# Kernel tuning notes

Hardware: AMD Instinct MI355X
Metric: run time of the kernel (lower is better)

## Reference

```python
import jax, jax.numpy as jnp
import numpy as np


def setup_inputs() -> dict:
    key = jax.random.key(0)
    ks = jax.random.split(key, 7)
    B, D, K, L = 32768, 256, 8, 4
    s = 1.0 / np.sqrt(D)
    return {
        "x": jax.random.normal(ks[0], (B, D), jnp.float32),
        "gate_W": jax.random.normal(ks[1], (D, K), jnp.float32) * s,
        "gate_b": jax.random.normal(ks[2], (K,), jnp.float32) * s,
        "block_W": jax.random.normal(ks[3], (L, K, D, D), jnp.float32) * s,
        "block_b": jax.random.normal(ks[4], (L, K, D), jnp.float32) * s,
        "out_W": jax.random.normal(ks[5], (K, D, D), jnp.float32) * s,
        "out_b": jax.random.normal(ks[6], (K, D), jnp.float32) * s,
    }


def _moie_block(x, alpha, W, b):
    # x: (B, in), alpha: (B, K), W: (K, in, out), b: (K, out)
    z = jnp.einsum('bi,kio->bko', x, W) + b[None]        # (B, K, out)
    return jnp.einsum('bk,bko->bo', alpha, z)            # alpha-weighted sum over experts


def reference(x, gate_W, gate_b, block_W, block_b, out_W, out_b):
    # standard gating: softmax(Linear(x)); same alpha reused at every layer
    alpha = jax.nn.softmax(x @ gate_W + gate_b, axis=-1)  # (B, K)
    h = x
    num_layers = block_W.shape[0]
    for i in range(num_layers):
        h = jax.nn.relu(_moie_block(h, alpha, block_W[i], block_b[i]))
    # output block, no activation
    return _moie_block(h, alpha, out_W, out_b)
```

## Files before the change

kernel.cpp:

```cpp
#include <hip/hip_runtime.h>
#include <hip/hip_bf16.h>

typedef __attribute__((ext_vector_type(8))) _Float16 h8v;
typedef __attribute__((ext_vector_type(4))) float f4v;

__device__ __forceinline__ ushort f16bits(float f) {
    _Float16 h = (_Float16)f;
    return __builtin_bit_cast(unsigned short, h);
}

#define GL2LDS16(g, l) __builtin_amdgcn_global_load_lds( \
    (const __attribute__((address_space(1))) void*)(g),  \
    (__attribute__((address_space(3))) void*)(l), 16, 0, 0)

#define VMCNT4() asm volatile("s_waitcnt vmcnt(4)" ::: "memory")
#define VMCNT0() asm volatile("s_waitcnt vmcnt(0)" ::: "memory")
#define LGKM0()  asm volatile("s_waitcnt lgkmcnt(0)" ::: "memory")
#define BAR()    asm volatile("s_barrier" ::: "memory")

__global__ __launch_bounds__(256) void gate_kernel(
    const float* __restrict__ x, const float* __restrict__ gW,
    const float* __restrict__ gb, float* __restrict__ alpha)
{
    int lane = threadIdx.x & 63;
    int wave = threadIdx.x >> 6;
    int row = blockIdx.x * 4 + wave;
    float4 xv = *(const float4*)(x + (size_t)row * 256 + lane * 4);
    const float* xp = (const float*)&xv;
    float p[8];
#pragma unroll
    for (int k = 0; k < 8; ++k) p[k] = 0.f;
#pragma unroll
    for (int j = 0; j < 4; ++j) {
        float xs = xp[j];
        const float* wr = gW + (lane * 4 + j) * 8;
#pragma unroll
        for (int k = 0; k < 8; ++k) p[k] = fmaf(xs, wr[k], p[k]);
    }
#pragma unroll
    for (int off = 32; off > 0; off >>= 1) {
#pragma unroll
        for (int k = 0; k < 8; ++k) p[k] += __shfl_xor(p[k], off);
    }
    float m = -1e30f;
#pragma unroll
    for (int k = 0; k < 8; ++k) { p[k] += gb[k]; m = fmaxf(m, p[k]); }
    float s = 0.f;
#pragma unroll
    for (int k = 0; k < 8; ++k) { p[k] = expf(p[k] - m); s += p[k]; }
    if (lane < 8) alpha[(size_t)row * 8 + lane] = p[lane] / s;
}

__global__ __launch_bounds__(256) void prep_weights(
    const float* __restrict__ blockW, const float* __restrict__ outW,
    ushort* __restrict__ Wh)
{
    int mat = blockIdx.x >> 4;
    int tile = blockIdx.x & 15;
    int i0 = (tile >> 2) * 64, o0 = (tile & 3) * 64;
    const float* src = (mat < 32) ? (blockW + (size_t)mat * 65536)
                                  : (outW + (size_t)(mat - 32) * 65536);
    __shared__ float tl[64][65];
    int r = threadIdx.x >> 2, c0 = (threadIdx.x & 3) * 16;
#pragma unroll
    for (int e = 0; e < 16; e += 4) {
        float4 v = *(const float4*)(src + (size_t)(i0 + r) * 256 + o0 + c0 + e);
        tl[r][c0 + e + 0] = v.x; tl[r][c0 + e + 1] = v.y;
        tl[r][c0 + e + 2] = v.z; tl[r][c0 + e + 3] = v.w;
    }
    __syncthreads();
    int oc = threadIdx.x >> 2, ic0 = (threadIdx.x & 3) * 16;
    uint hp[8];
#pragma unroll
    for (int e = 0; e < 16; e += 2) {
        ushort h0 = f16bits(tl[ic0 + e][oc]);
        ushort h1 = f16bits(tl[ic0 + e + 1][oc]);
        hp[e >> 1] = (uint)h0 | ((uint)h1 << 16);
    }
    size_t base = ((size_t)(mat * 256 + o0 + oc)) * 256 + i0 + ic0;
    *(uint4*)(Wh + base)     = make_uint4(hp[0], hp[1], hp[2], hp[3]);
    *(uint4*)(Wh + base + 8) = make_uint4(hp[4], hp[5], hp[6], hp[7]);
}

template<bool RELU>
__global__ __launch_bounds__(256, 2) void moie_gemm(
    const float* __restrict__ Hin, float* __restrict__ Hout,
    const ushort* __restrict__ Wh,
    const float* __restrict__ bias, const float* __restrict__ alpha)
{
    __shared__ __align__(16) ushort Ah[64 * 256];
    __shared__ __align__(16) ushort Bh[2][256 * 32];

    const int tid  = threadIdx.x;
    const int lane = tid & 63;
    const int wid  = tid >> 6;
    const int m0   = blockIdx.x * 64;
    const int wcol0 = wid * 64;
    const int kgl = lane >> 4;
    const int fr  = lane & 15;

    float areg[4][8];
#pragma unroll
    for (int im = 0; im < 4; ++im) {
        const float4* ap = (const float4*)(alpha + (size_t)(m0 + im * 16 + fr) * 8);
        float4 a0 = ap[0], a1 = ap[1];
        areg[im][0] = a0.x; areg[im][1] = a0.y; areg[im][2] = a0.z; areg[im][3] = a0.w;
        areg[im][4] = a1.x; areg[im][5] = a1.y; areg[im][6] = a1.z; areg[im][7] = a1.w;
    }

    int bgoff[4];
#pragma unroll
    for (int q = 0; q < 4; ++q) {
        int c = q * 256 + tid;
        int n = c >> 2;
        int kg = (c & 3) ^ ((n >> 1) & 3);
        bgoff[q] = n * 256 + kg * 8;
    }
    int boff[4];
#pragma unroll
    for (int in = 0; in < 4; ++in) {
        int n = wcol0 + in * 16 + fr;
        boff[in] = n * 32 + (kgl ^ ((n >> 1) & 3)) * 8;
    }

#pragma unroll
    for (int q = 0; q < 4; ++q)
        GL2LDS16(Wh + bgoff[q], &Bh[0][(q * 256 + wid * 64) * 8]);

    {
        const int r0  = tid >> 6;
        const int kk  = (tid & 63) * 4;
        const int kg  = kk >> 3;
        const int klo = kk & 7;
#pragma unroll
        for (int p = 0; p < 16; ++p) {
            int row = p * 4 + r0;
            float4 v = *(const float4*)(Hin + (size_t)(m0 + row) * 256 + kk);
            uint2 pk;
            pk.x = (uint)f16bits(v.x) | ((uint)f16bits(v.y) << 16);
            pk.y = (uint)f16bits(v.z) | ((uint)f16bits(v.w) << 16);
            *(uint2*)&Ah[row * 256 + (kg ^ (row & 7)) * 8 + klo] = pk;
        }
    }
    LGKM0();

    f4v acc[4][4];
#pragma unroll
    for (int a = 0; a < 4; ++a)
#pragma unroll
        for (int b = 0; b < 4; ++b) acc[a][b] = (f4v){0.f, 0.f, 0.f, 0.f};

    h8v afc[4];

#pragma unroll 1
    for (int t = 0; t < 64; ++t) {
        const int cur = t & 1;
        if (t < 63) {
            const int tn  = t + 1;
            const int en  = tn & 7;
            const int ki0 = (tn >> 3) * 32;
#pragma unroll
            for (int q = 0; q < 4; ++q)
                GL2LDS16(Wh + (size_t)en * 65536 + bgoff[q] + ki0,
                         &Bh[cur ^ 1][(q * 256 + wid * 64) * 8]);
            VMCNT4();
        } else {
            VMCNT0();
        }
        BAR();
        if ((t & 7) == 0) {
            const int kg0 = (t >> 3) * 4;
#pragma unroll
            for (int im = 0; im < 4; ++im) {
                int row = im * 16 + fr;
                afc[im] = *(const h8v*)&Ah[row * 256 + ((kg0 + kgl) ^ (row & 7)) * 8];
            }
        }
        const int e = t & 7;
        h8v as[4];
#pragma unroll
        for (int im = 0; im < 4; ++im) {
            _Float16 ah = (_Float16)areg[im][e];
            as[im] = afc[im] * ah;
        }
        h8v bf[4];
#pragma unroll
        for (int in = 0; in < 4; ++in)
            bf[in] = *(const h8v*)&Bh[cur][boff[in]];
        __builtin_amdgcn_s_setprio(1);
#pragma unroll
        for (int im = 0; im < 4; ++im)
#pragma unroll
            for (int in = 0; in < 4; ++in)
                acc[im][in] = __builtin_amdgcn_mfma_f32_16x16x32_f16(as[im], bf[in], acc[im][in], 0, 0, 0);
        __builtin_amdgcn_s_setprio(0);
        BAR();
    }

    float bv[4][8];
#pragma unroll
    for (int in = 0; in < 4; ++in) {
        int col = wcol0 + in * 16 + fr;
#pragma unroll
        for (int k = 0; k < 8; ++k) bv[in][k] = bias[k * 256 + col];
    }
#pragma unroll
    for (int im = 0; im < 4; ++im) {
#pragma unroll
        for (int j = 0; j < 4; ++j) {
            int row = m0 + im * 16 + kgl * 4 + j;
            const float4* ap = (const float4*)(alpha + (size_t)row * 8);
            float4 a0 = ap[0], a1 = ap[1];
            float a8[8] = {a0.x, a0.y, a0.z, a0.w, a1.x, a1.y, a1.z, a1.w};
#pragma unroll
            for (int in = 0; in < 4; ++in) {
                int col = wcol0 + in * 16 + fr;
                float be = 0.f;
#pragma unroll
                for (int k = 0; k < 8; ++k) be = fmaf(a8[k], bv[in][k], be);
                float v = acc[im][in][j] + be;
                if (RELU) v = fmaxf(v, 0.f);
                Hout[(size_t)row * 256 + col] = v;
            }
        }
    }
}

extern "C" void kernel_launch(void* const* d_in, const int* in_sizes, int n_in,
                              void* d_out, int out_size, void* d_ws, size_t ws_size,
                              hipStream_t stream)
{
    const float* x      = (const float*)d_in[0];
    const float* gW     = (const float*)d_in[1];
    const float* gb     = (const float*)d_in[2];
    const float* blockW = (const float*)d_in[3];
    const float* blockB = (const float*)d_in[4];
    const float* outW   = (const float*)d_in[5];
    const float* outB   = (const float*)d_in[6];
    float* out = (float*)d_out;

    char* ws = (char*)d_ws;
    float*  alpha = (float*)ws;
    ushort* Wh    = (ushort*)(ws + (1 << 20));

    prep_weights<<<640, 256, 0, stream>>>(blockW, outW, Wh);
    gate_kernel<<<8192, 256, 0, stream>>>(x, gW, gb, alpha);

    const size_t WL = (size_t)8 * 65536;
    moie_gemm<true ><<<512, 256, 0, stream>>>(x,   out, Wh,          blockB,            alpha);
    moie_gemm<true ><<<512, 256, 0, stream>>>(out, out, Wh + 1 * WL, blockB + 1 * 2048, alpha);
    moie_gemm<true ><<<512, 256, 0, stream>>>(out, out, Wh + 2 * WL, blockB + 2 * 2048, alpha);
    moie_gemm<true ><<<512, 256, 0, stream>>>(out, out, Wh + 3 * WL, blockB + 3 * 2048, alpha);
    moie_gemm<false><<<512, 256, 0, stream>>>(out, out, Wh + 4 * WL, outB,              alpha);
}
```

Measured before the change: 298.8 us.

## Restructure MoIE GEMM to 128-row blocks, fp16 activations, and register-held A

Each GEMM block now covers 128 rows with 512 threads (8 waves in a 2x4 grid), so every loaded weight tile is reused across twice as many rows. K is staged in 64-wide slices instead of 32, which halves the number of barrier steps. Activations are loaded straight from global into registers per K-slice instead of through an LDS tile. Intermediate layers are stored as fp16 to cut activation traffic, and two MFMA/LDS interleaving variants alternate across layers. The costs are higher register pressure and an in-place fp16 read/write of the same buffer, which stays safe only because each block reads its own rows before writing them.

```diff
diff --git a/kernel.cpp b/kernel.cpp
--- a/kernel.cpp
+++ b/kernel.cpp
@@ -15,7 +15,6 @@
 
 #define VMCNT4() asm volatile("s_waitcnt vmcnt(4)" ::: "memory")
 #define VMCNT0() asm volatile("s_waitcnt vmcnt(0)" ::: "memory")
-#define LGKM0()  asm volatile("s_waitcnt lgkmcnt(0)" ::: "memory")
 #define BAR()    asm volatile("s_barrier" ::: "memory")
 
 __global__ __launch_bounds__(256) void gate_kernel(
@@ -82,119 +81,147 @@
     *(uint4*)(Wh + base + 8) = make_uint4(hp[4], hp[5], hp[6], hp[7]);
 }
 
-template<bool RELU>
-__global__ __launch_bounds__(256, 2) void moie_gemm(
-    const float* __restrict__ Hin, float* __restrict__ Hout,
-    const ushort* __restrict__ Wh,
-    const float* __restrict__ bias, const float* __restrict__ alpha)
-{
-    __shared__ __align__(16) ushort Ah[64 * 256];
-    __shared__ __align__(16) ushort Bh[2][256 * 32];
+template<int VARIANT, bool F32IN, bool LAST>
+__global__ __launch_bounds__(512, 2) void moie_gemm(
+    const void* __restrict__ HinV, ushort* __restrict__ Hout16,
+    float* __restrict__ HoutF,
+    const ushort* __restrict__ Wh, const float* __restrict__ bias,
+    const float* __restrict__ alpha)
+{
+    __shared__ __align__(16) ushort Bh[2][256 * 64];
 
     const int tid  = threadIdx.x;
     const int lane = tid & 63;
     const int wid  = tid >> 6;
-    const int m0   = blockIdx.x * 64;
-    const int wcol0 = wid * 64;
+    const int wr   = wid >> 2;
+    const int wc   = wid & 3;
+    const int m0   = blockIdx.x * 128;
+    const int row0 = m0 + wr * 64;
+    const int wcol0 = wc * 64;
     const int kgl = lane >> 4;
     const int fr  = lane & 15;
 
-    float areg[4][8];
+    const ushort* Hin16 = (const ushort*)HinV;
+    const float*  HinF  = (const float*)HinV;
+
+    _Float16 ah[4][8];
 #pragma unroll
     for (int im = 0; im < 4; ++im) {
-        const float4* ap = (const float4*)(alpha + (size_t)(m0 + im * 16 + fr) * 8);
+        const float4* ap = (const float4*)(alpha + (size_t)(row0 + im * 16 + fr) * 8);
         float4 a0 = ap[0], a1 = ap[1];
-        areg[im][0] = a0.x; areg[im][1] = a0.y; areg[im][2] = a0.z; areg[im][3] = a0.w;
-        areg[im][4] = a1.x; areg[im][5] = a1.y; areg[im][6] = a1.z; areg[im][7] = a1.w;
-    }
-
-    int bgoff[4];
+        ah[im][0] = (_Float16)a0.x; ah[im][1] = (_Float16)a0.y;
+        ah[im][2] = (_Float16)a0.z; ah[im][3] = (_Float16)a0.w;
+        ah[im][4] = (_Float16)a1.x; ah[im][5] = (_Float16)a1.y;
+        ah[im][6] = (_Float16)a1.z; ah[im][7] = (_Float16)a1.w;
+    }
+
+    int soff[4];
 #pragma unroll
     for (int q = 0; q < 4; ++q) {
-        int c = q * 256 + tid;
-        int n = c >> 2;
-        int kg = (c & 3) ^ ((n >> 1) & 3);
-        bgoff[q] = n * 256 + kg * 8;
-    }
-    int boff[4];
+        int n = q * 64 + (tid >> 3);
+        int kgp = tid & 7;
+        soff[q] = n * 256 + ((kgp ^ (n & 7)) << 3);
+    }
+    int boff[4][2];
 #pragma unroll
     for (int in = 0; in < 4; ++in) {
         int n = wcol0 + in * 16 + fr;
-        boff[in] = n * 32 + (kgl ^ ((n >> 1) & 3)) * 8;
+#pragma unroll
+        for (int ks = 0; ks < 2; ++ks)
+            boff[in][ks] = n * 64 + (((ks * 4 + kgl) ^ (n & 7)) << 3);
     }
 
 #pragma unroll
     for (int q = 0; q < 4; ++q)
-        GL2LDS16(Wh + bgoff[q], &Bh[0][(q * 256 + wid * 64) * 8]);
-
-    {
-        const int r0  = tid >> 6;
-        const int kk  = (tid & 63) * 4;
-        const int kg  = kk >> 3;
-        const int klo = kk & 7;
-#pragma unroll
-        for (int p = 0; p < 16; ++p) {
-            int row = p * 4 + r0;
-            float4 v = *(const float4*)(Hin + (size_t)(m0 + row) * 256 + kk);
-            uint2 pk;
-            pk.x = (uint)f16bits(v.x) | ((uint)f16bits(v.y) << 16);
-            pk.y = (uint)f16bits(v.z) | ((uint)f16bits(v.w) << 16);
-            *(uint2*)&Ah[row * 256 + (kg ^ (row & 7)) * 8 + klo] = pk;
+        GL2LDS16(Wh + soff[q], &Bh[0][q * 4096 + wid * 512]);
+
+    f4v acc[4][4];
+#pragma unroll
+    for (int a = 0; a < 4; ++a)
+#pragma unroll
+        for (int b = 0; b < 4; ++b) acc[a][b] = (f4v){0.f, 0.f, 0.f, 0.f};
+
+    h8v afc[4][2];
+
+#pragma unroll 1
+    for (int kt = 0; kt < 4; ++kt) {
+#pragma unroll
+        for (int im = 0; im < 4; ++im) {
+            const size_t rb = (size_t)(row0 + im * 16 + fr) * 256 + kt * 64 + kgl * 8;
+#pragma unroll
+            for (int ks = 0; ks < 2; ++ks) {
+                if (F32IN) {
+                    float4 v0 = *(const float4*)(HinF + rb + ks * 32);
+                    float4 v1 = *(const float4*)(HinF + rb + ks * 32 + 4);
+                    h8v tv;
+                    tv[0] = (_Float16)v0.x; tv[1] = (_Float16)v0.y;
+                    tv[2] = (_Float16)v0.z; tv[3] = (_Float16)v0.w;
+                    tv[4] = (_Float16)v1.x; tv[5] = (_Float16)v1.y;
+                    tv[6] = (_Float16)v1.z; tv[7] = (_Float16)v1.w;
+                    afc[im][ks] = tv;
+                } else {
+                    afc[im][ks] = *(const h8v*)(Hin16 + rb + ks * 32);
+                }
+            }
         }
-    }
-    LGKM0();
-
-    f4v acc[4][4];
-#pragma unroll
-    for (int a = 0; a < 4; ++a)
-#pragma unroll
-        for (int b = 0; b < 4; ++b) acc[a][b] = (f4v){0.f, 0.f, 0.f, 0.f};
-
-    h8v afc[4];
-
-#pragma unroll 1
-    for (int t = 0; t < 64; ++t) {
-        const int cur = t & 1;
-        if (t < 63) {
-            const int tn  = t + 1;
-            const int en  = tn & 7;
-            const int ki0 = (tn >> 3) * 32;
-#pragma unroll
-            for (int q = 0; q < 4; ++q)
-                GL2LDS16(Wh + (size_t)en * 65536 + bgoff[q] + ki0,
-                         &Bh[cur ^ 1][(q * 256 + wid * 64) * 8]);
-            VMCNT4();
-        } else {
-            VMCNT0();
+#pragma unroll
+        for (int e = 0; e < 8; ++e) {
+            const int t   = kt * 8 + e;
+            const int cur = t & 1;
+            if (t < 31) {
+                const int ne  = (e < 7) ? e + 1 : 0;
+                const int nkt = (e < 7) ? kt : kt + 1;
+                const ushort* src = Wh + (size_t)ne * 65536 + nkt * 64;
+#pragma unroll
+                for (int q = 0; q < 4; ++q)
+                    GL2LDS16(src + soff[q], &Bh[cur ^ 1][q * 4096 + wid * 512]);
+                VMCNT4();
+            } else {
+                VMCNT0();
+            }
+            BAR();
+            h8v as[4][2];
+#pragma unroll
+            for (int im = 0; im < 4; ++im)
+#pragma unroll
+                for (int ks = 0; ks < 2; ++ks)
+                    as[im][ks] = afc[im][ks] * ah[im][e];
+            if (VARIANT == 0) {
+                h8v bf[4][2];
+#pragma unroll
+                for (int in = 0; in < 4; ++in)
+#pragma unroll
+                    for (int ks = 0; ks < 2; ++ks)
+                        bf[in][ks] = *(const h8v*)&Bh[cur][boff[in][ks]];
+                __builtin_amdgcn_s_setprio(1);
+#pragma unroll
+                for (int im = 0; im < 4; ++im)
+#pragma unroll
+                    for (int in = 0; in < 4; ++in)
+#pragma unroll
+                        for (int ks = 0; ks < 2; ++ks)
+                            acc[im][in] = __builtin_amdgcn_mfma_f32_16x16x32_f16(
+                                as[im][ks], bf[in][ks], acc[im][in], 0, 0, 0);
+                __builtin_amdgcn_s_setprio(0);
+                BAR();
+            } else {
+#pragma unroll
+                for (int p = 0; p < 4; ++p) {
+                    h8v b0 = *(const h8v*)&Bh[cur][boff[p][0]];
+                    h8v b1 = *(const h8v*)&Bh[cur][boff[p][1]];
+                    __builtin_amdgcn_s_setprio(1);
+#pragma unroll
+                    for (int im = 0; im < 4; ++im) {
+                        acc[im][p] = __builtin_amdgcn_mfma_f32_16x16x32_f16(
+                            as[im][0], b0, acc[im][p], 0, 0, 0);
+                        acc[im][p] = __builtin_amdgcn_mfma_f32_16x16x32_f16(
+                            as[im][1], b1, acc[im][p], 0, 0, 0);
+                    }
+                    __builtin_amdgcn_s_setprio(0);
+                    BAR();
+                }
+            }
         }
-        BAR();
-        if ((t & 7) == 0) {
-            const int kg0 = (t >> 3) * 4;
-#pragma unroll
-            for (int im = 0; im < 4; ++im) {
-                int row = im * 16 + fr;
-                afc[im] = *(const h8v*)&Ah[row * 256 + ((kg0 + kgl) ^ (row & 7)) * 8];
-            }
-        }
-        const int e = t & 7;
-        h8v as[4];
-#pragma unroll
-        for (int im = 0; im < 4; ++im) {
-            _Float16 ah = (_Float16)areg[im][e];
-            as[im] = afc[im] * ah;
-        }
-        h8v bf[4];
-#pragma unroll
-        for (int in = 0; in < 4; ++in)
-            bf[in] = *(const h8v*)&Bh[cur][boff[in]];
-        __builtin_amdgcn_s_setprio(1);
-#pragma unroll
-        for (int im = 0; im < 4; ++im)
-#pragma unroll
-            for (int in = 0; in < 4; ++in)
-                acc[im][in] = __builtin_amdgcn_mfma_f32_16x16x32_f16(as[im], bf[in], acc[im][in], 0, 0, 0);
-        __builtin_amdgcn_s_setprio(0);
-        BAR();
     }
 
     float bv[4][8];
@@ -208,7 +235,7 @@
     for (int im = 0; im < 4; ++im) {
 #pragma unroll
         for (int j = 0; j < 4; ++j) {
-            int row = m0 + im * 16 + kgl * 4 + j;
+            int row = row0 + im * 16 + kgl * 4 + j;
             const float4* ap = (const float4*)(alpha + (size_t)row * 8);
             float4 a0 = ap[0], a1 = ap[1];
             float a8[8] = {a0.x, a0.y, a0.z, a0.w, a1.x, a1.y, a1.z, a1.w};
@@ -219,8 +246,12 @@
 #pragma unroll
                 for (int k = 0; k < 8; ++k) be = fmaf(a8[k], bv[in][k], be);
                 float v = acc[im][in][j] + be;
-                if (RELU) v = fmaxf(v, 0.f);
-                Hout[(size_t)row * 256 + col] = v;
+                if (LAST) {
+                    HoutF[(size_t)row * 256 + col] = v;
+                } else {
+                    v = fmaxf(v, 0.f);
+                    Hout16[(size_t)row * 256 + col] = f16bits(v);
+                }
             }
         }
     }
@@ -242,14 +273,15 @@
     char* ws = (char*)d_ws;
     float*  alpha = (float*)ws;
     ushort* Wh    = (ushort*)(ws + (1 << 20));
+    ushort* H16   = (ushort*)(ws + (8 << 20));
 
     prep_weights<<<640, 256, 0, stream>>>(blockW, outW, Wh);
     gate_kernel<<<8192, 256, 0, stream>>>(x, gW, gb, alpha);
 
     const size_t WL = (size_t)8 * 65536;
-    moie_gemm<true ><<<512, 256, 0, stream>>>(x,   out, Wh,          blockB,            alpha);
-    moie_gemm<true ><<<512, 256, 0, stream>>>(out, out, Wh + 1 * WL, blockB + 1 * 2048, alpha);
-    moie_gemm<true ><<<512, 256, 0, stream>>>(out, out, Wh + 2 * WL, blockB + 2 * 2048, alpha);
-    moie_gemm<true ><<<512, 256, 0, stream>>>(out, out, Wh + 3 * WL, blockB + 3 * 2048, alpha);
-    moie_gemm<false><<<512, 256, 0, stream>>>(out, out, Wh + 4 * WL, outB,              alpha);
-}
+    moie_gemm<1, true , false><<<256, 512, 0, stream>>>(x,   H16, nullptr, Wh,          blockB,            alpha);
+    moie_gemm<0, false, false><<<256, 512, 0, stream>>>(H16, H16, nullptr, Wh + 1 * WL, blockB + 1 * 2048, alpha);
+    moie_gemm<1, false, false><<<256, 512, 0, stream>>>(H16, H16, nullptr, Wh + 2 * WL, blockB + 2 * 2048, alpha);
+    moie_gemm<0, false, false><<<256, 512, 0, stream>>>(H16, H16, nullptr, Wh + 3 * WL, blockB + 3 * 2048, alpha);
+    moie_gemm<1, false, true ><<<256, 512, 0, stream>>>(H16, nullptr, out, Wh + 4 * WL, outB,              alpha);
+}
```

Measured after the change: 734.6 us. 146% more time.
